# Kernel optimization log

Measured on AMD Instinct MI355X. Metric: run time of the kernel, lower is better.

## Reference

```python
import jax, jax.numpy as jnp
import numpy as np

B, L, F, DM, H, DFF, NL, PRED = 8, 1000, 7, 512, 8, 2048, 4, 50
DK = DM // H           # head dim 64
P = DK // 4            # learned-mask proj dim 16
EPS = 1e-5
SCALE = 1.0 / float(np.sqrt(DK))


def _ln(x, g, b):
    m = jnp.mean(x, -1, keepdims=True)
    v = jnp.mean((x - m) ** 2, -1, keepdims=True)
    return (x - m) / jnp.sqrt(v + EPS) * g + b


def _make_pe():
    pos = np.arange(L, dtype=np.float32)[:, None]
    div = np.exp(np.arange(0, DM, 2, dtype=np.float32) * (-np.log(10000.0) / DM))
    pe = np.zeros((L, DM), dtype=np.float32)
    pe[:, 0::2] = np.sin(pos * div)
    pe[:, 1::2] = np.cos(pos * div)
    return jnp.asarray(pe)


def setup_inputs() -> dict:
    key = jax.random.key(0)
    ks = iter(jax.random.split(key, 40))
    def w(shape, s=0.02):
        return jax.random.normal(next(ks), shape, jnp.float32) * s
    return {
        "x": jax.random.normal(next(ks), (B, L, F), jnp.float32),
        "emb_w": w((F, DM)), "emb_b": jnp.zeros((DM,), jnp.float32),
        "pe": _make_pe(),
        "Wq": w((NL, DM, DM)), "bq": jnp.zeros((NL, DM), jnp.float32),
        "Wk": w((NL, DM, DM)), "bk": jnp.zeros((NL, DM), jnp.float32),
        "Wv": w((NL, DM, DM)), "bv": jnp.zeros((NL, DM), jnp.float32),
        "Wo": w((NL, DM, DM)), "bo": jnp.zeros((NL, DM), jnp.float32),
        "W1": w((NL, DM, DFF)), "b1": jnp.zeros((NL, DFF), jnp.float32),
        "W2": w((NL, DFF, DM)), "b2": jnp.zeros((NL, DM), jnp.float32),
        "g1": jnp.ones((NL, DM), jnp.float32), "be1": jnp.zeros((NL, DM), jnp.float32),
        "g2": jnp.ones((NL, DM), jnp.float32), "be2": jnp.zeros((NL, DM), jnp.float32),
        "lm_qw": w((DK, P)), "lm_qb": jnp.zeros((P,), jnp.float32),
        "lm_kw": w((DK, P)), "lm_kb": jnp.zeros((P,), jnp.float32),
        "gn": jnp.ones((DM,), jnp.float32), "bn": jnp.zeros((DM,), jnp.float32),
        "fc_w": w((DM, PRED)), "fc_b": jnp.zeros((PRED,), jnp.float32),
    }


def reference(x, emb_w, emb_b, pe, Wq, bq, Wk, bk, Wv, bv, Wo, bo,
              W1, b1, W2, b2, g1, be1, g2, be2,
              lm_qw, lm_qb, lm_kw, lm_kb, gn, bn, fc_w, fc_b):
    # eval mode: dropout = identity
    h = x @ emb_w + emb_b + pe[None]                 # [B,L,DM]
    for i in range(NL):
        q = (h @ Wq[i] + bq[i]).reshape(B, L, H, DK)
        k = (h @ Wk[i] + bk[i]).reshape(B, L, H, DK)
        v = (h @ Wv[i] + bv[i]).reshape(B, L, H, DK)
        scores = jnp.einsum('blhd,bshd->bhls', q, k) * SCALE
        # shared LearnedMask: per-head Q/K projection to P dims, tanh bias
        qp = q @ lm_qw + lm_qb                       # [B,L,H,P]
        kp = k @ lm_kw + lm_kb                       # [B,S,H,P]
        scores = scores + jnp.tanh(jnp.einsum('blhp,bshp->bhls', qp, kp))
        attn = jax.nn.softmax(scores, axis=-1)       # mask_flag=False: no mask
        ctx = jnp.einsum('bhls,bshd->blhd', attn, v).reshape(B, L, DM)
        h = _ln(h + ctx @ Wo[i] + bo[i], g1[i], be1[i])
        y = jax.nn.relu(h @ W1[i] + b1[i]) @ W2[i] + b2[i]
        h2 = _ln(h + y, g2[i], be2[i])
        h = _ln(h2 + y, g2[i], be2[i])               # module applies norm2 twice
    h = _ln(h, gn, bn)                               # Encoder final norm
    return h[:, -1, :] @ fc_w + fc_b                 # [B, PRED]
```

## Files before the change

### kernel.cpp

```cpp
#include <hip/hip_runtime.h>
#include <math.h>

#define B_    8
#define L_    1000
#define F_    7
#define DM_   512
#define H_    8
#define DFF_  2048
#define NL_   4
#define PRED_ 50
#define DK_   64
#define P_    16
#define EPS_  1e-5f
#define QKVS  1792

#define L2E_   1.4426950408889634f
#define C_QS   0.18033688011112042f
#define BS_QP  2.8853900817779268f
#define SHFT_  24.0f

typedef unsigned short u16;
typedef __bf16 bf16x8 __attribute__((ext_vector_type(8)));
typedef float  f32x4  __attribute__((ext_vector_type(4)));

__device__ inline float wave_reduce_sum(float x) {
#pragma unroll
  for (int off = 32; off >= 1; off >>= 1) x += __shfl_xor(x, off, 64);
  return x;
}
__device__ inline u16 f2bf(float f) {
  unsigned int u = __float_as_uint(f);
  unsigned int r = u + 0x7FFFu + ((u >> 16) & 1u);
  return (u16)(r >> 16);
}
__device__ inline unsigned int pack2(float a, float b) {
  return (unsigned int)f2bf(a) | ((unsigned int)f2bf(b) << 16);
}
__device__ inline float bf2f(u16 u) { return __uint_as_float(((unsigned int)u) << 16); }
__device__ inline float fexp2(float x) { return __builtin_amdgcn_exp2f(x); }
__device__ inline float frcp(float x) { return __builtin_amdgcn_rcpf(x); }

union bfrag { bf16x8 b; uint4 q; u16 u[8]; };

__device__ inline void gload16(const u16* g, u16* l) {
  __builtin_amdgcn_global_load_lds(
      (const __attribute__((address_space(1))) void*)g,
      (__attribute__((address_space(3))) void*)l, 16, 0, 0);
}

__global__ __launch_bounds__(256)
void transpose_w(const float* __restrict__ in, u16* __restrict__ out,
                 int K, int N, size_t in_lstride, size_t out_lstride,
                 int row_off, int out_ld) {
  __shared__ float tile[32][33];
  int z = blockIdx.z;
  int kk0 = blockIdx.y * 32, nn0 = blockIdx.x * 32;
  int tx = threadIdx.x & 31, ty = threadIdx.x >> 5;
  const float* ip = in + z * in_lstride;
  u16* op = out + z * out_lstride;
#pragma unroll
  for (int i = 0; i < 4; i++)
    tile[ty + i * 8][tx] = ip[(size_t)(kk0 + ty + i * 8) * N + nn0 + tx];
  __syncthreads();
#pragma unroll
  for (int i = 0; i < 4; i++)
    op[(size_t)(row_off + nn0 + ty + i * 8) * out_ld + kk0 + tx] = f2bf(tile[tx][ty + i * 8]);
}

__global__ __launch_bounds__(256)
void wfuse_kernel(const float* __restrict__ Wq, const float* __restrict__ Wk,
                  const float* __restrict__ lmqw, const float* __restrict__ lmkw,
                  u16* __restrict__ Wt) {
  int hh = blockIdx.x, side = blockIdx.y, layer = blockIdx.z;
  const float* W = (side ? Wk : Wq) + (size_t)layer * 512 * 512;
  const float* lw = side ? lmkw : lmqw;
  float scale = side ? 1.0f : BS_QP;
  __shared__ float lws[64][17];
  int t = threadIdx.x;
  for (int i = t; i < 1024; i += 256) lws[i >> 4][i & 15] = lw[i];
  __syncthreads();
  int p = t & 15, kk = t >> 4;
  u16* orow = Wt + (size_t)layer * QKVS * 512 + (size_t)(1536 + side * 128 + hh * 16 + p) * 512;
  for (int kb = 0; kb < 32; kb++) {
    int k = kb * 16 + kk;
    const float* wr = W + (size_t)k * 512 + hh * 64;
    float acc = 0.f;
#pragma unroll
    for (int d = 0; d < 64; d++) acc = fmaf(wr[d], lws[d][p], acc);
    orow[k] = f2bf(acc * scale);
  }
}

__global__ __launch_bounds__(256)
void concat_bias(const float* __restrict__ bq, const float* __restrict__ bk,
                 const float* __restrict__ bv,
                 const float* __restrict__ lmqw, const float* __restrict__ lmqb,
                 const float* __restrict__ lmkw, const float* __restrict__ lmkb,
                 float* __restrict__ bqkv) {
  int i = blockIdx.x * 256 + threadIdx.x;
  int l = i / QKVS, j = i % QKVS;
  float v;
  if (j < 512) v = bq[l * 512 + j];
  else if (j < 1024) v = bk[l * 512 + j - 512];
  else if (j < 1536) v = bv[l * 512 + j - 1024];
  else if (j < 1664) {
    int hh = (j - 1536) >> 4, p = (j - 1536) & 15;
    float acc = lmqb[p];
#pragma unroll
    for (int d = 0; d < 64; d++) acc = fmaf(bq[l * 512 + hh * 64 + d], lmqw[d * 16 + p], acc);
    v = acc * BS_QP;
  } else {
    int hh = (j - 1664) >> 4, p = (j - 1664) & 15;
    float acc = lmkb[p];
#pragma unroll
    for (int d = 0; d < 64; d++) acc = fmaf(bk[l * 512 + hh * 64 + d], lmkw[d * 16 + p], acc);
    v = acc;
  }
  bqkv[i] = v;
}

__global__ __launch_bounds__(512)
void embed_kernel(const float* __restrict__ x, const float* __restrict__ emb_w,
                  const float* __restrict__ emb_b, const float* __restrict__ pe,
                  u16* __restrict__ h16) {
  int bl = blockIdx.x;
  int l = bl % L_;
  int d = threadIdx.x;
  const float* xr = x + (size_t)bl * F_;
  float acc = emb_b[d] + pe[(size_t)l * DM_ + d];
#pragma unroll
  for (int f = 0; f < F_; f++) acc = fmaf(xr[f], emb_w[f * DM_ + d], acc);
  h16[(size_t)bl * DM_ + d] = f2bf(acc);
}

template<int BN>
__global__ __launch_bounds__(256)
void gemm16(const u16* __restrict__ A, const u16* __restrict__ Bt,
            const float* __restrict__ bias, const u16* __restrict__ resid,
            u16* __restrict__ C16, u16* __restrict__ vtg,
            int M, int K, int N, int relu, int nscale, float sval) {
  constexpr int NTW = BN / 32;
  constexpr int BG  = BN / 32;
  constexpr int ASZ = 128 * 64;
  constexpr int BSZ = BN * 64;
  __shared__ u16 As[2 * ASZ];
  __shared__ u16 Bs[2 * BSZ];
  int t = threadIdx.x;
  int w = t >> 6, lane = t & 63;
  int wr = w >> 1, wc = w & 1;
  int mloc = lane & 15, quad = lane >> 4;
  int m0 = blockIdx.y * 128, n0 = blockIdx.x * BN;

  const u16* agp[4]; u16* alds[4];
#pragma unroll
  for (int j = 0; j < 4; j++) {
    int r = w * 32 + j * 8 + (lane >> 3);
    int gm = m0 + r; if (gm > M - 1) gm = M - 1;
    int ch = (lane & 7) ^ (r & 7);
    agp[j] = A + (size_t)gm * K + ch * 8;
    alds[j] = As + (w * 32 + j * 8) * 64;
  }
  const u16* bgp[BG]; u16* blds[BG];
#pragma unroll
  for (int j = 0; j < BG; j++) {
    int r = w * (8 * BG) + j * 8 + (lane >> 3);
    int ch = (lane & 7) ^ (r & 7);
    bgp[j] = Bt + (size_t)(n0 + r) * K + ch * 8;
    blds[j] = Bs + (w * (8 * BG) + j * 8) * 64;
  }
  const u16* apt[2][4];
#pragma unroll
  for (int mi = 0; mi < 4; mi++) {
    int tr = wr * 64 + mi * 16 + mloc;
    apt[0][mi] = As + tr * 64 + ((quad ^ (tr & 7)) * 8);
    apt[1][mi] = As + tr * 64 + (((4 + quad) ^ (tr & 7)) * 8);
  }
  const u16* bpt[2][NTW];
#pragma unroll
  for (int nt = 0; nt < NTW; nt++) {
    int tr = wc * (BN / 2) + nt * 16 + mloc;
    bpt[0][nt] = Bs + tr * 64 + ((quad ^ (tr & 7)) * 8);
    bpt[1][nt] = Bs + tr * 64 + (((4 + quad) ^ (tr & 7)) * 8);
  }

  f32x4 acc[4][NTW];
#pragma unroll
  for (int mi = 0; mi < 4; mi++)
#pragma unroll
    for (int nt = 0; nt < NTW; nt++) acc[mi][nt] = (f32x4){0.f, 0.f, 0.f, 0.f};

#pragma unroll
  for (int j = 0; j < 4; j++) gload16(agp[j], alds[j]);
#pragma unroll
  for (int j = 0; j < BG; j++) gload16(bgp[j], blds[j]);
  __syncthreads();

  const int nk = K >> 6;
  int cur = 0;
  for (int tt = 0; tt < nk; ++tt) {
    if (tt + 1 < nk) {
      const int nxt = cur ^ 1;
      const int koff = (tt + 1) * 64;
#pragma unroll
      for (int j = 0; j < 4; j++) gload16(agp[j] + koff, alds[j] + nxt * ASZ);
#pragma unroll
      for (int j = 0; j < BG; j++) gload16(bgp[j] + koff, blds[j] + nxt * BSZ);
    }
    const int ao = cur * ASZ, bo = cur * BSZ;
#pragma unroll
    for (int kc = 0; kc < 2; kc++) {
      bf16x8 af[4], bv[NTW];
#pragma unroll
      for (int mi = 0; mi < 4; mi++) af[mi] = *(const bf16x8*)(apt[kc][mi] + ao);
#pragma unroll
      for (int nt = 0; nt < NTW; nt++) bv[nt] = *(const bf16x8*)(bpt[kc][nt] + bo);
#pragma unroll
      for (int mi = 0; mi < 4; mi++)
#pragma unroll
        for (int nt = 0; nt < NTW; nt++)
          acc[mi][nt] = __builtin_amdgcn_mfma_f32_16x16x32_bf16(af[mi], bv[nt], acc[mi][nt], 0, 0, 0);
    }
    if (tt + 1 < nk) __syncthreads();
    cur ^= 1;
  }

#pragma unroll
  for (int mi = 0; mi < 4; mi++) {
    int m_r0 = m0 + wr * 64 + mi * 16 + quad * 4;
#pragma unroll
    for (int nt = 0; nt < NTW; nt++) {
      int nbase = n0 + wc * (BN / 2) + nt * 16;
      int n = nbase + mloc;
      if (vtg && nbase >= 1024 && nbase < 1536) {
        if (m_r0 < M) {
          int bb = (m_r0 * 67109) >> 26;
          int ll = m_r0 - bb * 1000;
          int hh2 = (n - 1024) >> 6, dk = n & 63;
          float bn_ = bias[n];
          union { uint2 d; u16 s[4]; } pk;
#pragma unroll
          for (int r = 0; r < 4; r++) pk.s[r] = f2bf(acc[mi][nt][r] + bn_);
          u16* dst = vtg + ((size_t)(bb * 8 + hh2) * 64 + dk) * 1024 + ll;
          *(uint2*)dst = pk.d;
        }
      } else {
        float bn_ = bias[n];
#pragma unroll
        for (int r = 0; r < 4; r++) {
          int m = m_r0 + r;
          if (m >= M) continue;
          size_t crow = (size_t)m * N;
          float vsum = acc[mi][nt][r] + bn_;
          if (resid) vsum += bf2f(resid[crow + n]);
          if (n < nscale) vsum *= sval;
          if (relu) vsum = fmaxf(vsum, 0.f);
          C16[crow + n] = f2bf(vsum);
        }
      }
    }
  }
}

#define KT   64
#define KPLD 24
#define PSLD 40
__global__ __launch_bounds__(256)
void attn_mfma_kernel(const u16* __restrict__ qkv, const u16* __restrict__ vtg,
                      u16* __restrict__ ctx) {
  __shared__ u16 Ks[KT * 64];
  __shared__ u16 Vt[64 * KT];
  __shared__ u16 Kp[KT * KPLD];
  __shared__ u16 Ps[4 * 16 * PSLD];

  int Lid = blockIdx.x;
  int qt = Lid >> 6;
  int bh = ((Lid & 7) << 3) | ((Lid >> 3) & 7);
  int b = bh >> 3, hh = bh & 7;
  int l0 = qt * 64;
  int t = threadIdx.x;
  int wv = t >> 6, lane = t & 63;
  int m = lane & 15, quad = lane >> 4;

  int lq = l0 + wv * 16 + m; if (lq > L_ - 1) lq = L_ - 1;
  const u16* qrow = qkv + (size_t)(b * L_ + lq) * QKVS + hh * DK_;
  bf16x8 qa0 = *(const bf16x8*)(qrow + quad * 8);
  bf16x8 qa1 = *(const bf16x8*)(qrow + 32 + quad * 8);
  bfrag qpa;
  if (quad < 2) {
    qpa.q = *(const uint4*)(qkv + (size_t)(b * L_ + lq) * QKVS + 1536 + hh * P_ + quad * 8);
  } else {
    qpa.q = make_uint4(0u, 0u, 0u, 0u);
  }

  const u16* ks_g = qkv + ((size_t)b * L_ + (t >> 3)) * QKVS + 512 + hh * DK_
                    + ((t & 7) ^ ((t >> 3) & 7)) * 8;
  u16* ks_l = Ks + (t >> 6) * 512;
  const u16* vt_g = vtg + ((size_t)bh * DK_ + (t >> 3)) * 1024
                    + ((t & 7) ^ ((t >> 3) & 7)) * 8;
  u16* vt_l = Vt + (t >> 6) * 512;

  f32x4 O[4];
#pragma unroll
  for (int nt = 0; nt < 4; nt++) O[nt] = (f32x4){0.f, 0.f, 0.f, 0.f};
  float lrun[4] = {0.f, 0.f, 0.f, 0.f};

  u16* pw = Ps + wv * (16 * PSLD);
  const u16* pr0 = pw + m * PSLD + quad * 8;
  const f32x4 zz = (f32x4){0.f, 0.f, 0.f, 0.f};

  for (int s0 = 0; s0 < L_; s0 += KT) {
    uint4 p0, p1;
    if (t < KT) {
      int sg2 = s0 + t; if (sg2 > L_ - 1) sg2 = L_ - 1;
      const u16* pr = qkv + (size_t)(b * L_ + sg2) * QKVS + 1664 + hh * P_;
      p0 = *(const uint4*)(pr);
      p1 = *(const uint4*)(pr + 8);
    }
    __syncthreads();
#pragma unroll
    for (int j = 0; j < 2; j++) {
      gload16(ks_g + ((size_t)s0 + j * 32) * QKVS, ks_l + j * 2048);
      gload16(vt_g + s0 + (size_t)j * 32 * 1024, vt_l + j * 2048);
    }
    if (t < KT) {
      *(uint4*)&Kp[t * KPLD]     = p0;
      *(uint4*)&Kp[t * KPLD + 8] = p1;
    }
    __syncthreads();

#pragma unroll
    for (int kc = 0; kc < 2; kc++) {
      float pv2[2][4];
#pragma unroll
      for (int h2 = 0; h2 < 2; h2++) {
        int nt = kc * 2 + h2;
        const u16* kb = Ks + (nt * 16 + m) * 64;
        int x0 = ((quad) ^ (m & 7)) * 8;
        int x1 = ((4 + quad) ^ (m & 7)) * 8;
        __builtin_amdgcn_s_setprio(1);
        f32x4 sacc = __builtin_amdgcn_mfma_f32_16x16x32_bf16(qa0, *(const bf16x8*)(kb + x0), zz, 0, 0, 0);
        sacc = __builtin_amdgcn_mfma_f32_16x16x32_bf16(qa1, *(const bf16x8*)(kb + x1), sacc, 0, 0, 0);
        bf16x8 kpf = *(const bf16x8*)(Kp + (nt * 16 + m) * KPLD + (quad & 1) * 8);
        f32x4 macc = __builtin_amdgcn_mfma_f32_16x16x32_bf16(qpa.b, kpf, zz, 0, 0, 0);
        __builtin_amdgcn_s_setprio(0);
        bool oob = (s0 + nt * 16 + m) >= L_;
#pragma unroll
        for (int r = 0; r < 4; r++) {
          float e = fexp2(macc[r]);
          float d = frcp(e + 1.f);
          float th = fmaf(d, -2.f * L2E_, L2E_);
          float s = sacc[r] + th;
          if (oob) s = -3e38f;
          float p = fexp2(s - SHFT_);
          pv2[h2][r] = p;
          lrun[r] += p;
        }
      }
#pragma unroll
      for (int h2 = 0; h2 < 2; h2++)
#pragma unroll
        for (int r = 0; r < 4; r++)
          pw[(quad * 4 + r) * PSLD + h2 * 16 + m] = f2bf(pv2[h2][r]);
      bf16x8 pa = *(const bf16x8*)pr0;
      __builtin_amdgcn_s_setprio(1);
#pragma unroll
      for (int ntd = 0; ntd < 4; ntd++) {
        const u16* vb = Vt + (ntd * 16 + m) * KT + (((kc * 4 + quad) ^ (m & 7)) * 8);
        O[ntd] = __builtin_amdgcn_mfma_f32_16x16x32_bf16(pa, *(const bf16x8*)vb, O[ntd], 0, 0, 0);
      }
      __builtin_amdgcn_s_setprio(0);
    }
  }

  float inv[4];
#pragma unroll
  for (int r = 0; r < 4; r++) {
#pragma unroll
    for (int msk = 1; msk < 16; msk <<= 1) lrun[r] += __shfl_xor(lrun[r], msk, 64);
    inv[r] = frcp(lrun[r]);
  }
#pragma unroll
  for (int r = 0; r < 4; r++) {
    int l = l0 + wv * 16 + quad * 4 + r;
    if (l >= L_) continue;
    u16* crow = ctx + ((size_t)(b * L_ + l)) * DM_ + hh * DK_;
#pragma unroll
    for (int nt = 0; nt < 4; nt++) crow[nt * 16 + m] = f2bf(O[nt][r] * inv[r]);
  }
}

__global__ __launch_bounds__(256)
void ln_kernel(const u16* __restrict__ a, const float* __restrict__ g,
               const float* __restrict__ be, u16* __restrict__ o) {
  int row = blockIdx.x;
  int t = threadIdx.x;
  size_t base = (size_t)row * DM_;
  unsigned int av = *(const unsigned int*)(a + base + 2 * t);
  float x0 = bf2f((u16)av), x1 = bf2f((u16)(av >> 16));
  float s = wave_reduce_sum(x0 + x1);
  float ss = wave_reduce_sum(x0 * x0 + x1 * x1);
  __shared__ float sh_s[4], sh_ss[4];
  int wv = t >> 6, lane = t & 63;
  if (lane == 0) { sh_s[wv] = s; sh_ss[wv] = ss; }
  __syncthreads();
  float S = sh_s[0] + sh_s[1] + sh_s[2] + sh_s[3];
  float SS = sh_ss[0] + sh_ss[1] + sh_ss[2] + sh_ss[3];
  float mean = S * (1.0f / DM_);
  float var = SS * (1.0f / DM_) - mean * mean;
  float rstd = rsqrtf(var + EPS_);
  float r0 = (x0 - mean) * rstd * g[2 * t] + be[2 * t];
  float r1 = (x1 - mean) * rstd * g[2 * t + 1] + be[2 * t + 1];
  *(unsigned int*)(o + base + 2 * t) = pack2(r0, r1);
}

__global__ __launch_bounds__(256)
void ln2x_kernel(const u16* __restrict__ hin, const u16* __restrict__ y,
                 const float* __restrict__ g, const float* __restrict__ be,
                 u16* __restrict__ o16) {
  int row = blockIdx.x;
  int t = threadIdx.x;
  size_t base = (size_t)row * DM_;
  unsigned int hv = *(const unsigned int*)(hin + base + 2 * t);
  unsigned int yv = *(const unsigned int*)(y + base + 2 * t);
  float y0 = bf2f((u16)yv), y1 = bf2f((u16)(yv >> 16));
  float x0 = bf2f((u16)hv) + y0, x1 = bf2f((u16)(hv >> 16)) + y1;
  __shared__ float sh_s[4], sh_ss[4];
  int wv = t >> 6, lane = t & 63;
  float g0 = g[2 * t], g1v = g[2 * t + 1], b0 = be[2 * t], b1v = be[2 * t + 1];

  float s = wave_reduce_sum(x0 + x1);
  float ss = wave_reduce_sum(x0 * x0 + x1 * x1);
  if (lane == 0) { sh_s[wv] = s; sh_ss[wv] = ss; }
  __syncthreads();
  float S = sh_s[0] + sh_s[1] + sh_s[2] + sh_s[3];
  float SS = sh_ss[0] + sh_ss[1] + sh_ss[2] + sh_ss[3];
  float mean = S * (1.0f / DM_);
  float var = SS * (1.0f / DM_) - mean * mean;
  float rstd = rsqrtf(var + EPS_);
  float h20 = (x0 - mean) * rstd * g0 + b0 + y0;
  float h21 = (x1 - mean) * rstd * g1v + b1v + y1;
  __syncthreads();

  s = wave_reduce_sum(h20 + h21);
  ss = wave_reduce_sum(h20 * h20 + h21 * h21);
  if (lane == 0) { sh_s[wv] = s; sh_ss[wv] = ss; }
  __syncthreads();
  S = sh_s[0] + sh_s[1] + sh_s[2] + sh_s[3];
  SS = sh_ss[0] + sh_ss[1] + sh_ss[2] + sh_ss[3];
  mean = S * (1.0f / DM_);
  var = SS * (1.0f / DM_) - mean * mean;
  rstd = rsqrtf(var + EPS_);
  float r0 = (h20 - mean) * rstd * g0 + b0;
  float r1 = (h21 - mean) * rstd * g1v + b1v;
  *(unsigned int*)(o16 + base + 2 * t) = pack2(r0, r1);
}

__global__ __launch_bounds__(512)
void final_kernel(const u16* __restrict__ h, const float* __restrict__ gn,
                  const float* __restrict__ bn, const float* __restrict__ fcw,
                  const float* __restrict__ fcb, float* __restrict__ out) {
  int b = blockIdx.x;
  int t = threadIdx.x;
  size_t base = ((size_t)b * L_ + (L_ - 1)) * DM_;
  float x = bf2f(h[base + t]);
  float s = wave_reduce_sum(x);
  float ss = wave_reduce_sum(x * x);
  __shared__ float sh_s[8], sh_ss[8];
  int wv = t >> 6, lane = t & 63;
  if (lane == 0) { sh_s[wv] = s; sh_ss[wv] = ss; }
  __syncthreads();
  float S = 0.f, SS = 0.f;
#pragma unroll
  for (int i = 0; i < 8; i++) { S += sh_s[i]; SS += sh_ss[i]; }
  float mean = S * (1.0f / DM_);
  float var = SS * (1.0f / DM_) - mean * mean;
  float rstd = rsqrtf(var + EPS_);
  __shared__ float hn[DM_];
  hn[t] = (x - mean) * rstd * gn[t] + bn[t];
  __syncthreads();
  if (t < PRED_) {
    float acc = fcb[t];
#pragma unroll 8
    for (int d = 0; d < DM_; d++) acc = fmaf(hn[d], fcw[d * PRED_ + t], acc);
    out[b * PRED_ + t] = acc;
  }
}

extern "C" void kernel_launch(void* const* d_in, const int* in_sizes, int n_in,
                              void* d_out, int out_size, void* d_ws, size_t ws_size,
                              hipStream_t stream) {
  const float* x     = (const float*)d_in[0];
  const float* emb_w = (const float*)d_in[1];
  const float* emb_b = (const float*)d_in[2];
  const float* pe    = (const float*)d_in[3];
  const float* Wq = (const float*)d_in[4];  const float* bq = (const float*)d_in[5];
  const float* Wk = (const float*)d_in[6];  const float* bk = (const float*)d_in[7];
  const float* Wv = (const float*)d_in[8];  const float* bv = (const float*)d_in[9];
  const float* Wo = (const float*)d_in[10]; const float* bo = (const float*)d_in[11];
  const float* W1 = (const float*)d_in[12]; const float* b1 = (const float*)d_in[13];
  const float* W2 = (const float*)d_in[14]; const float* b2 = (const float*)d_in[15];
  const float* g1 = (const float*)d_in[16]; const float* be1 = (const float*)d_in[17];
  const float* g2 = (const float*)d_in[18]; const float* be2 = (const float*)d_in[19];
  const float* lm_qw = (const float*)d_in[20]; const float* lm_qb = (const float*)d_in[21];
  const float* lm_kw = (const float*)d_in[22]; const float* lm_kb = (const float*)d_in[23];
  const float* gn = (const float*)d_in[24]; const float* bn = (const float*)d_in[25];
  const float* fc_w = (const float*)d_in[26]; const float* fc_b = (const float*)d_in[27];
  float* out = (float*)d_out;

  const size_t ROWS = (size_t)B_ * L_;
  u16* qkv16 = (u16*)d_ws;
  u16* ctx16 = qkv16 + ROWS * QKVS;
  u16* ffn1  = qkv16;
  u16* h16   = ctx16 + ROWS * DM_;
  u16* t16   = h16 + ROWS * DM_;
  u16* vtg   = t16 + ROWS * DM_;
  u16* Wqkv_t = vtg + (size_t)64 * 64 * 1024;
  u16* Wo_t   = Wqkv_t + (size_t)NL_ * QKVS * DM_;
  u16* W1_t   = Wo_t + (size_t)NL_ * DM_ * DM_;
  u16* W2_t   = W1_t + (size_t)NL_ * DFF_ * DM_;
  float* bqkv = (float*)(W2_t + (size_t)NL_ * DM_ * DFF_);

  transpose_w<<<dim3(16, 16, NL_), 256, 0, stream>>>(Wq, Wqkv_t, DM_, DM_, (size_t)DM_ * DM_, (size_t)QKVS * DM_, 0, DM_);
  transpose_w<<<dim3(16, 16, NL_), 256, 0, stream>>>(Wk, Wqkv_t, DM_, DM_, (size_t)DM_ * DM_, (size_t)QKVS * DM_, 512, DM_);
  transpose_w<<<dim3(16, 16, NL_), 256, 0, stream>>>(Wv, Wqkv_t, DM_, DM_, (size_t)DM_ * DM_, (size_t)QKVS * DM_, 1024, DM_);
  transpose_w<<<dim3(16, 16, NL_), 256, 0, stream>>>(Wo, Wo_t, DM_, DM_, (size_t)DM_ * DM_, (size_t)DM_ * DM_, 0, DM_);
  transpose_w<<<dim3(64, 16, NL_), 256, 0, stream>>>(W1, W1_t, DM_, DFF_, (size_t)DM_ * DFF_, (size_t)DFF_ * DM_, 0, DM_);
  transpose_w<<<dim3(16, 64, NL_), 256, 0, stream>>>(W2, W2_t, DFF_, DM_, (size_t)DFF_ * DM_, (size_t)DM_ * DFF_, 0, DFF_);
  wfuse_kernel<<<dim3(H_, 2, NL_), 256, 0, stream>>>(Wq, Wk, lm_qw, lm_kw, Wqkv_t);
  concat_bias<<<NL_ * QKVS / 256, 256, 0, stream>>>(bq, bk, bv, lm_qw, lm_qb, lm_kw, lm_kb, bqkv);

  embed_kernel<<<dim3((unsigned)ROWS), 512, 0, stream>>>(x, emb_w, emb_b, pe, h16);

  dim3 g_qkv(QKVS / 128, 63);
  dim3 g_ffn1(DFF_ / 128, 63);
  dim3 g_n512(DM_ / 64, 63);
  dim3 g_attn(1024);

  for (int i = 0; i < NL_; i++) {
    gemm16<128><<<g_qkv, 256, 0, stream>>>(h16, Wqkv_t + (size_t)i * QKVS * DM_,
        bqkv + i * QKVS, nullptr, qkv16, vtg, 8000, DM_, QKVS, 0, 512, C_QS);

    attn_mfma_kernel<<<g_attn, 256, 0, stream>>>(qkv16, vtg, ctx16);

    gemm16<64><<<g_n512, 256, 0, stream>>>(ctx16, Wo_t + (size_t)i * DM_ * DM_,
        bo + i * DM_, h16, t16, nullptr, 8000, DM_, DM_, 0, 0, 1.0f);
    ln_kernel<<<dim3((unsigned)ROWS), 256, 0, stream>>>(t16, g1 + i * DM_, be1 + i * DM_, h16);

    gemm16<128><<<g_ffn1, 256, 0, stream>>>(h16, W1_t + (size_t)i * DFF_ * DM_,
        b1 + i * DFF_, nullptr, ffn1, nullptr, 8000, DM_, DFF_, 1, 0, 1.0f);
    gemm16<64><<<g_n512, 256, 0, stream>>>(ffn1, W2_t + (size_t)i * DM_ * DFF_,
        b2 + i * DM_, nullptr, t16, nullptr, 8000, DFF_, DM_, 0, 0, 1.0f);

    ln2x_kernel<<<dim3((unsigned)ROWS), 256, 0, stream>>>(h16, t16, g2 + i * DM_, be2 + i * DM_, h16);
  }

  final_kernel<<<B_, 512, 0, stream>>>(h16, gn, bn, fc_w, fc_b, out);
}
```

Measured before the change: 1.136 ms.

## Shrink GEMM tiles to 64 rows with K=32 steps; make layernorm one wave per row

The GEMM kernel now uses 64-row M tiles and 32-wide K slices, with a re-swizzled LDS layout that packs two rows per 64-element line. The M grid roughly doubles, so more blocks are available across the many CUs. This costs less operand reuse per block and twice as many K iterations and barriers. The layernorm kernels now handle one row per wavefront with 8 elements per lane and shuffle-only reductions, removing the LDS round trips and block barriers.

```diff
diff --git a/kernel.cpp b/kernel.cpp
--- a/kernel.cpp
+++ b/kernel.cpp
@@ -135,98 +135,92 @@
 
 template<int BN>
 __global__ __launch_bounds__(256)
-void gemm16(const u16* __restrict__ A, const u16* __restrict__ Bt,
+void gemm64(const u16* __restrict__ A, const u16* __restrict__ Bt,
             const float* __restrict__ bias, const u16* __restrict__ resid,
             u16* __restrict__ C16, u16* __restrict__ vtg,
             int M, int K, int N, int relu, int nscale, float sval) {
   constexpr int NTW = BN / 32;
-  constexpr int BG  = BN / 32;
-  constexpr int ASZ = 128 * 64;
-  constexpr int BSZ = BN * 64;
+  constexpr int BG  = BN / 64;
+  constexpr int ASZ = 32 * 64;
+  constexpr int BSZ = (BN / 2) * 64;
   __shared__ u16 As[2 * ASZ];
   __shared__ u16 Bs[2 * BSZ];
   int t = threadIdx.x;
   int w = t >> 6, lane = t & 63;
   int wr = w >> 1, wc = w & 1;
   int mloc = lane & 15, quad = lane >> 4;
-  int m0 = blockIdx.y * 128, n0 = blockIdx.x * BN;
-
-  const u16* agp[4]; u16* alds[4];
-#pragma unroll
-  for (int j = 0; j < 4; j++) {
-    int r = w * 32 + j * 8 + (lane >> 3);
-    int gm = m0 + r; if (gm > M - 1) gm = M - 1;
-    int ch = (lane & 7) ^ (r & 7);
-    agp[j] = A + (size_t)gm * K + ch * 8;
-    alds[j] = As + (w * 32 + j * 8) * 64;
+  int m0 = blockIdx.y * 64, n0 = blockIdx.x * BN;
+
+  const u16* agp; u16* alds;
+  {
+    int R = w * 8 + (lane >> 3);
+    int c = (lane & 7) ^ (R & 7);
+    int gm = m0 + 2 * R + (c >> 2); if (gm > M - 1) gm = M - 1;
+    agp = A + (size_t)gm * K + (c & 3) * 8;
+    alds = As + (w * 8) * 64;
   }
   const u16* bgp[BG]; u16* blds[BG];
 #pragma unroll
   for (int j = 0; j < BG; j++) {
-    int r = w * (8 * BG) + j * 8 + (lane >> 3);
-    int ch = (lane & 7) ^ (r & 7);
-    bgp[j] = Bt + (size_t)(n0 + r) * K + ch * 8;
+    int R = w * (8 * BG) + j * 8 + (lane >> 3);
+    int c = (lane & 7) ^ (R & 7);
+    bgp[j] = Bt + (size_t)(n0 + 2 * R + (c >> 2)) * K + (c & 3) * 8;
     blds[j] = Bs + (w * (8 * BG) + j * 8) * 64;
   }
-  const u16* apt[2][4];
-#pragma unroll
-  for (int mi = 0; mi < 4; mi++) {
-    int tr = wr * 64 + mi * 16 + mloc;
-    apt[0][mi] = As + tr * 64 + ((quad ^ (tr & 7)) * 8);
-    apt[1][mi] = As + tr * 64 + (((4 + quad) ^ (tr & 7)) * 8);
-  }
-  const u16* bpt[2][NTW];
+  const u16* apt[2];
+#pragma unroll
+  for (int mi = 0; mi < 2; mi++) {
+    int tr = wr * 32 + mi * 16 + mloc;
+    int R = tr >> 1, c = (tr & 1) * 4 + quad;
+    apt[mi] = As + R * 64 + ((c ^ (R & 7)) * 8);
+  }
+  const u16* bpt[NTW];
 #pragma unroll
   for (int nt = 0; nt < NTW; nt++) {
     int tr = wc * (BN / 2) + nt * 16 + mloc;
-    bpt[0][nt] = Bs + tr * 64 + ((quad ^ (tr & 7)) * 8);
-    bpt[1][nt] = Bs + tr * 64 + (((4 + quad) ^ (tr & 7)) * 8);
-  }
-
-  f32x4 acc[4][NTW];
-#pragma unroll
-  for (int mi = 0; mi < 4; mi++)
+    int R = tr >> 1, c = (tr & 1) * 4 + quad;
+    bpt[nt] = Bs + R * 64 + ((c ^ (R & 7)) * 8);
+  }
+
+  f32x4 acc[2][NTW];
+#pragma unroll
+  for (int mi = 0; mi < 2; mi++)
 #pragma unroll
     for (int nt = 0; nt < NTW; nt++) acc[mi][nt] = (f32x4){0.f, 0.f, 0.f, 0.f};
 
-#pragma unroll
-  for (int j = 0; j < 4; j++) gload16(agp[j], alds[j]);
+  gload16(agp, alds);
 #pragma unroll
   for (int j = 0; j < BG; j++) gload16(bgp[j], blds[j]);
   __syncthreads();
 
-  const int nk = K >> 6;
+  const int nk = K >> 5;
   int cur = 0;
   for (int tt = 0; tt < nk; ++tt) {
     if (tt + 1 < nk) {
       const int nxt = cur ^ 1;
-      const int koff = (tt + 1) * 64;
-#pragma unroll
-      for (int j = 0; j < 4; j++) gload16(agp[j] + koff, alds[j] + nxt * ASZ);
+      const int koff = (tt + 1) * 32;
+      gload16(agp + koff, alds + nxt * ASZ);
 #pragma unroll
       for (int j = 0; j < BG; j++) gload16(bgp[j] + koff, blds[j] + nxt * BSZ);
     }
     const int ao = cur * ASZ, bo = cur * BSZ;
-#pragma unroll
-    for (int kc = 0; kc < 2; kc++) {
-      bf16x8 af[4], bv[NTW];
-#pragma unroll
-      for (int mi = 0; mi < 4; mi++) af[mi] = *(const bf16x8*)(apt[kc][mi] + ao);
-#pragma unroll
-      for (int nt = 0; nt < NTW; nt++) bv[nt] = *(const bf16x8*)(bpt[kc][nt] + bo);
-#pragma unroll
-      for (int mi = 0; mi < 4; mi++)
-#pragma unroll
-        for (int nt = 0; nt < NTW; nt++)
-          acc[mi][nt] = __builtin_amdgcn_mfma_f32_16x16x32_bf16(af[mi], bv[nt], acc[mi][nt], 0, 0, 0);
-    }
+    bf16x8 af[2], bv[NTW];
+#pragma unroll
+    for (int mi = 0; mi < 2; mi++) af[mi] = *(const bf16x8*)(apt[mi] + ao);
+#pragma unroll
+    for (int nt = 0; nt < NTW; nt++) bv[nt] = *(const bf16x8*)(bpt[nt] + bo);
+#pragma unroll
+    for (int mi = 0; mi < 2; mi++)
+#pragma unroll
+      for (int nt = 0; nt < NTW; nt++)
+        acc[mi][nt] = __builtin_amdgcn_mfma_f32_16x16x32_bf16(af[mi], bv[nt], acc[mi][nt], 0, 0, 0);
     if (tt + 1 < nk) __syncthreads();
     cur ^= 1;
   }
 
 #pragma unroll
-  for (int mi = 0; mi < 4; mi++) {
-    int m_r0 = m0 + wr * 64 + mi * 16 + quad * 4;
+  for (int mi = 0; mi < 2; mi++) {
+    int m_r0 = m0 + wr * 32 + mi * 16 + quad * 4;
 #pragma unroll
     for (int nt = 0; nt < NTW; nt++) {
       int nbase = n0 + wc * (BN / 2) + nt * 16;
@@ -392,67 +386,68 @@
 __global__ __launch_bounds__(256)
 void ln_kernel(const u16* __restrict__ a, const float* __restrict__ g,
                const float* __restrict__ be, u16* __restrict__ o) {
-  int row = blockIdx.x;
-  int t = threadIdx.x;
-  size_t base = (size_t)row * DM_;
-  unsigned int av = *(const unsigned int*)(a + base + 2 * t);
-  float x0 = bf2f((u16)av), x1 = bf2f((u16)(av >> 16));
-  float s = wave_reduce_sum(x0 + x1);
-  float ss = wave_reduce_sum(x0 * x0 + x1 * x1);
-  __shared__ float sh_s[4], sh_ss[4];
-  int wv = t >> 6, lane = t & 63;
-  if (lane == 0) { sh_s[wv] = s; sh_ss[wv] = ss; }
-  __syncthreads();
-  float S = sh_s[0] + sh_s[1] + sh_s[2] + sh_s[3];
-  float SS = sh_ss[0] + sh_ss[1] + sh_ss[2] + sh_ss[3];
-  float mean = S * (1.0f / DM_);
-  float var = SS * (1.0f / DM_) - mean * mean;
+  int wv = threadIdx.x >> 6, lane = threadIdx.x & 63;
+  int row = blockIdx.x * 4 + wv;
+  size_t base = (size_t)row * DM_ + lane * 8;
+  bfrag v; v.q = *(const uint4*)(a + base);
+  float x[8], s = 0.f, ss = 0.f;
+#pragma unroll
+  for (int i = 0; i < 8; i++) { x[i] = bf2f(v.u[i]); s += x[i]; ss = fmaf(x[i], x[i], ss); }
+#pragma unroll
+  for (int off = 32; off >= 1; off >>= 1) { s += __shfl_xor(s, off, 64); ss += __shfl_xor(ss, off, 64); }
+  float mean = s * (1.0f / DM_);
+  float var = ss * (1.0f / DM_) - mean * mean;
   float rstd = rsqrtf(var + EPS_);
-  float r0 = (x0 - mean) * rstd * g[2 * t] + be[2 * t];
-  float r1 = (x1 - mean) * rstd * g[2 * t + 1] + be[2 * t + 1];
-  *(unsigned int*)(o + base + 2 * t) = pack2(r0, r1);
+  float4 g0 = *(const float4*)(g + lane * 8), g1 = *(const float4*)(g + lane * 8 + 4);
+  float4 b0 = *(const float4*)(be + lane * 8), b1 = *(const float4*)(be + lane * 8 + 4);
+  float gv[8] = {g0.x, g0.y, g0.z, g0.w, g1.x, g1.y, g1.z, g1.w};
+  float bv[8] = {b0.x, b0.y, b0.z, b0.w, b1.x, b1.y, b1.z, b1.w};
+  bfrag r;
+#pragma unroll
+  for (int i = 0; i < 8; i++) r.u[i] = f2bf((x[i] - mean) * rstd * gv[i] + bv[i]);
+  *(uint4*)(o + base) = r.q;
 }
 
 __global__ __launch_bounds__(256)
 void ln2x_kernel(const u16* __restrict__ hin, const u16* __restrict__ y,
                  const float* __restrict__ g, const float* __restrict__ be,
                  u16* __restrict__ o16) {
-  int row = blockIdx.x;
-  int t = threadIdx.x;
-  size_t base = (size_t)row * DM_;
-  unsigned int hv = *(const unsigned int*)(hin + base + 2 * t);
-  unsigned int yv = *(const unsigned int*)(y + base + 2 * t);
-  float y0 = bf2f((u16)yv), y1 = bf2f((u16)(yv >> 16));
-  float x0 = bf2f((u16)hv) + y0, x1 = bf2f((u16)(hv >> 16)) + y1;
-  __shared__ float sh_s[4], sh_ss[4];
-  int wv = t >> 6, lane = t & 63;
-  float g0 = g[2 * t], g1v = g[2 * t + 1], b0 = be[2 * t], b1v = be[2 * t + 1];
-
-  float s = wave_reduce_sum(x0 + x1);
-  float ss = wave_reduce_sum(x0 * x0 + x1 * x1);
-  if (lane == 0) { sh_s[wv] = s; sh_ss[wv] = ss; }
-  __syncthreads();
-  float S = sh_s[0] + sh_s[1] + sh_s[2] + sh_s[3];
-  float SS = sh_ss[0] + sh_ss[1] + sh_ss[2] + sh_ss[3];
-  float mean = S * (1.0f / DM_);
-  float var = SS * (1.0f / DM_) - mean * mean;
+  int wv = threadIdx.x >> 6, lane = threadIdx.x & 63;
+  int row = blockIdx.x * 4 + wv;
+  size_t base = (size_t)row * DM_ + lane * 8;
+  bfrag hv; hv.q = *(const uint4*)(hin + base);
+  bfrag yv; yv.q = *(const uint4*)(y + base);
+  float4 g0 = *(const float4*)(g + lane * 8), g1 = *(const float4*)(g + lane * 8 + 4);
+  float4 b0 = *(const float4*)(be + lane * 8), b1 = *(const float4*)(be + lane * 8 + 4);
+  float gv[8] = {g0.x, g0.y, g0.z, g0.w, g1.x, g1.y, g1.z, g1.w};
+  float bv[8] = {b0.x, b0.y, b0.z, b0.w, b1.x, b1.y, b1.z, b1.w};
+  float x[8], yy[8], s = 0.f, ss = 0.f;
+#pragma unroll
+  for (int i = 0; i < 8; i++) {
+    yy[i] = bf2f(yv.u[i]);
+    x[i] = bf2f(hv.u[i]) + yy[i];
+    s += x[i]; ss = fmaf(x[i], x[i], ss);
+  }
+#pragma unroll
+  for (int off = 32; off >= 1; off >>= 1) { s += __shfl_xor(s, off, 64); ss += __shfl_xor(ss, off, 64); }
+  float mean = s * (1.0f / DM_);
+  float var = ss * (1.0f / DM_) - mean * mean;
   float rstd = rsqrtf(var + EPS_);
-  float h20 = (x0 - mean) * rstd * g0 + b0 + y0;
-  float h21 = (x1 - mean) * rstd * g1v + b1v + y1;
-  __syncthreads();
-
-  s = wave_reduce_sum(h20 + h21);
-  ss = wave_reduce_sum(h20 * h20 + h21 * h21);
-  if (lane == 0) { sh_s[wv] = s; sh_ss[wv] = ss; }
-  __syncthreads();
-  S = sh_s[0] + sh_s[1] + sh_s[2] + sh_s[3];
-  SS = sh_ss[0] + sh_ss[1] + sh_ss[2] + sh_ss[3];
-  mean = S * (1.0f / DM_);
-  var = SS * (1.0f / DM_) - mean * mean;
+  float h2[8]; s = 0.f; ss = 0.f;
+#pragma unroll
+  for (int i = 0; i < 8; i++) {
+    h2[i] = (x[i] - mean) * rstd * gv[i] + bv[i] + yy[i];
+    s += h2[i]; ss = fmaf(h2[i], h2[i], ss);
+  }
+#pragma unroll
+  for (int off = 32; off >= 1; off >>= 1) { s += __shfl_xor(s, off, 64); ss += __shfl_xor(ss, off, 64); }
+  mean = s * (1.0f / DM_);
+  var = ss * (1.0f / DM_) - mean * mean;
   rstd = rsqrtf(var + EPS_);
-  float r0 = (h20 - mean) * rstd * g0 + b0;
-  float r1 = (h21 - mean) * rstd * g1v + b1v;
-  *(unsigned int*)(o16 + base + 2 * t) = pack2(r0, r1);
+  bfrag r;
+#pragma unroll
+  for (int i = 0; i < 8; i++) r.u[i] = f2bf((h2[i] - mean) * rstd * gv[i] + bv[i]);
+  *(uint4*)(o16 + base) = r.q;
 }
 
 __global__ __launch_bounds__(512)
@@ -531,27 +526,28 @@
 
   embed_kernel<<<dim3((unsigned)ROWS), 512, 0, stream>>>(x, emb_w, emb_b, pe, h16);
 
-  dim3 g_qkv(QKVS / 128, 63);
-  dim3 g_ffn1(DFF_ / 128, 63);
-  dim3 g_n512(DM_ / 64, 63);
+  dim3 g_qkv(QKVS / 128, 125);
+  dim3 g_ffn1(DFF_ / 128, 125);
+  dim3 g_n512(DM_ / 64, 125);
   dim3 g_attn(1024);
+  dim3 g_ln(2000);
 
   for (int i = 0; i < NL_; i++) {
-    gemm16<128><<<g_qkv, 256, 0, stream>>>(h16, Wqkv_t + (size_t)i * QKVS * DM_,
+    gemm64<128><<<g_qkv, 256, 0, stream>>>(h16, Wqkv_t + (size_t)i * QKVS * DM_,
         bqkv + i * QKVS, nullptr, qkv16, vtg, 8000, DM_, QKVS, 0, 512, C_QS);
 
     attn_mfma_kernel<<<g_attn, 256, 0, stream>>>(qkv16, vtg, ctx16);
 
-    gemm16<64><<<g_n512, 256, 0, stream>>>(ctx16, Wo_t + (size_t)i * DM_ * DM_,
+    gemm64<64><<<g_n512, 256, 0, stream>>>(ctx16, Wo_t + (size_t)i * DM_ * DM_,
         bo + i * DM_, h16, t16, nullptr, 8000, DM_, DM_, 0, 0, 1.0f);
-    ln_kernel<<<dim3((unsigned)ROWS), 256, 0, stream>>>(t16, g1 + i * DM_, be1 + i * DM_, h16);
-
-    gemm16<128><<<g_ffn1, 256, 0, stream>>>(h16, W1_t + (size_t)i * DFF_ * DM_,
+    ln_kernel<<<g_ln, 256, 0, stream>>>(t16, g1 + i * DM_, be1 + i * DM_, h16);
+
+    gemm64<128><<<g_ffn1, 256, 0, stream>>>(h16, W1_t + (size_t)i * DFF_ * DM_,
         b1 + i * DFF_, nullptr, ffn1, nullptr, 8000, DM_, DFF_, 1, 0, 1.0f);
-    gemm16<64><<<g_n512, 256, 0, stream>>>(ffn1, W2_t + (size_t)i * DM_ * DFF_,
+    gemm64<64><<<g_n512, 256, 0, stream>>>(ffn1, W2_t + (size_t)i * DM_ * DFF_,
         b2 + i * DM_, nullptr, t16, nullptr, 8000, DFF_, DM_, 0, 0, 1.0f);
 
-    ln2x_kernel<<<dim3((unsigned)ROWS), 256, 0, stream>>>(h16, t16, g2 + i * DM_, be2 + i * DM_, h16);
+    ln2x_kernel<<<g_ln, 256, 0, stream>>>(h16, t16, g2 + i * DM_, be2 + i * DM_, h16);
   }
 
   final_kernel<<<B_, 512, 0, stream>>>(h16, gn, bn, fc_w, fc_b, out);
```

Result: faster. 1.033 ms (-9.1%).
